# Kernel tuning notes

Measured on AMD Instinct MI355X. Metric: run time of the kernel, lower is better.

The kernel has to match this reference:

```python
import jax, jax.numpy as jnp
import numpy as np

EMB = 128
HID = 256
VOCAB = 32000
B, LS, LT = 16, 256, 128


def _lstm(x_seq, h0, c0, Wk, Wr, b):
    """Keras-style LSTM (gate order i,f,g,o). x_seq: [B,T,D] -> ([B,T,H], h, c)."""
    xz = jnp.einsum('btd,dg->btg', x_seq, Wk) + b  # precompute input projection

    def step(carry, zt):
        h, c = carry
        z = zt + h @ Wr  # [B,4H]
        i, f, g, o = jnp.split(z, 4, axis=-1)
        c = jax.nn.sigmoid(f) * c + jax.nn.sigmoid(i) * jnp.tanh(g)
        h = jax.nn.sigmoid(o) * jnp.tanh(c)
        return (h, c), h

    (h, c), hs = jax.lax.scan(step, (h0, c0), xz.transpose(1, 0, 2))
    return hs.transpose(1, 0, 2), h, c


def setup_inputs() -> dict:
    key = jax.random.key(0)
    ks = jax.random.split(key, 12)
    sd_e = 1.0 / np.sqrt(EMB)
    sd_h = 1.0 / np.sqrt(HID)
    return {
        'x': jax.random.randint(ks[0], (B, LS), 0, VOCAB, dtype=jnp.int32),
        'y': jax.random.randint(ks[1], (B, LT), 0, VOCAB, dtype=jnp.int32),
        'enc_emb': jax.random.normal(ks[2], (VOCAB, EMB), jnp.float32) * 0.05,
        'enc_Wk': jax.random.normal(ks[3], (EMB, 4 * HID), jnp.float32) * sd_e,
        'enc_Wr': jax.random.normal(ks[4], (HID, 4 * HID), jnp.float32) * sd_h,
        'enc_b': jnp.zeros((4 * HID,), jnp.float32),
        'dec_emb': jax.random.normal(ks[5], (VOCAB, EMB), jnp.float32) * 0.05,
        'dec_Wk': jax.random.normal(ks[6], (EMB, 4 * HID), jnp.float32) * sd_e,
        'dec_Wr': jax.random.normal(ks[7], (HID, 4 * HID), jnp.float32) * sd_h,
        'dec_b': jnp.zeros((4 * HID,), jnp.float32),
        'Wout': jax.random.normal(ks[8], (2 * HID, VOCAB), jnp.float32) * (1.0 / np.sqrt(2 * HID)),
        'bout': jnp.zeros((VOCAB,), jnp.float32),
    }


def reference(x, y, enc_emb, enc_Wk, enc_Wr, enc_b, dec_emb, dec_Wk, dec_Wr, dec_b, Wout, bout):
    # ---- Encoder ----
    xe = enc_emb[x]  # [B,LS,EMB]
    z0 = jnp.zeros((x.shape[0], HID), jnp.float32)
    H, h, c = _lstm(xe, z0, z0, enc_Wk, enc_Wr, enc_b)  # H: [B,LS,HID]
    # ---- Decoder (teacher forcing) ----
    ye = dec_emb[y]  # [B,LT,EMB]
    S, hT, cT = _lstm(ye, h, c, dec_Wk, dec_Wr, dec_b)  # [B,LT,HID]
    S_ = jnp.concatenate([h[:, None, :], S[:, :-1, :]], axis=1)  # shifted states
    # Keras Attention (dot, no scale): A = softmax(S_ H^T) H
    scores = jnp.einsum('btd,bsd->bts', S_, H)  # [B,LT,LS]
    A = jnp.einsum('bts,bsd->btd', jax.nn.softmax(scores, axis=-1), H)
    feat = jnp.concatenate([S, A], axis=-1)  # [B,LT,2*HID]
    probs = jax.nn.softmax(feat @ Wout + bout, axis=-1)  # [B,LT,VOCAB]
    return probs
```

## Files before the change

### kernel.cpp

```cpp
#include <hip/hip_runtime.h>
#include <hip/hip_bf16.h>
#include <math.h>

#define BB    16
#define LS    256
#define LT    128
#define EMB   128
#define HID   256
#define G4    1024
#define VOCAB 32000

#define NSL   8
#define XROWS 112

typedef __attribute__((ext_vector_type(8))) short bf16x8;
typedef __attribute__((ext_vector_type(4))) float f32x4;
typedef __attribute__((ext_vector_type(4))) int   i32x4;
typedef unsigned short ushort_t;
typedef unsigned int uint_t;

__device__ inline float sigf(float x)      { return 1.0f / (1.0f + __expf(-x)); }
__device__ inline float tanhfast(float x)  { return 1.0f - 2.0f / (1.0f + __expf(2.0f * x)); }
__device__ inline ushort_t bf16_rne(float f) {
  __hip_bfloat16 h = __float2bfloat16(f);
  return *(ushort_t*)&h;
}

__global__ __launch_bounds__(256) void embed_proj_kernel(
    const int* __restrict__ x, const int* __restrict__ y,
    const float* __restrict__ eemb, const float* __restrict__ eWk,
    const float* __restrict__ eb,
    const float* __restrict__ demb, const float* __restrict__ dWk,
    const float* __restrict__ db,
    float* __restrict__ xze, float* __restrict__ xzd)
{
  const bool enc = blockIdx.x < 128;
  const int* idx = enc ? x : y;
  const float* emb = enc ? eemb : demb;
  const float* Wk  = enc ? eWk  : dWk;
  const float* bias= enc ? eb   : db;
  float* xz        = enc ? xze  : xzd;
  const int row0 = (enc ? blockIdx.x : blockIdx.x - 128) * 32;

  __shared__ float e[32][EMB];
  const int tid = threadIdx.x;

  for (int i = tid; i < 32 * EMB; i += 256) {
    int r = i >> 7, k = i & 127;
    int token = idx[row0 + r];
    e[r][k] = emb[(size_t)token * EMB + k];
  }
  __syncthreads();

  float acc[4][32];
#pragma unroll
  for (int q = 0; q < 4; ++q)
#pragma unroll
    for (int r = 0; r < 32; ++r) acc[q][r] = 0.0f;

  for (int k = 0; k < EMB; ++k) {
    float w0 = Wk[(size_t)k * G4 + 0 * 256 + tid];
    float w1 = Wk[(size_t)k * G4 + 1 * 256 + tid];
    float w2 = Wk[(size_t)k * G4 + 2 * 256 + tid];
    float w3 = Wk[(size_t)k * G4 + 3 * 256 + tid];
#pragma unroll
    for (int r = 0; r < 32; ++r) {
      float ev = e[r][k];
      acc[0][r] = fmaf(ev, w0, acc[0][r]);
      acc[1][r] = fmaf(ev, w1, acc[1][r]);
      acc[2][r] = fmaf(ev, w2, acc[2][r]);
      acc[3][r] = fmaf(ev, w3, acc[3][r]);
    }
  }
#pragma unroll
  for (int q = 0; q < 4; ++q) {
    float bb = bias[q * 256 + tid];
#pragma unroll
    for (int r = 0; r < 32; ++r)
      xz[(size_t)(row0 + r) * G4 + q * 256 + tid] = acc[q][r] + bb;
  }
}

__global__ __launch_bounds__(512, 1) void lstm_kernel(
    const float* __restrict__ xz,
    const float* __restrict__ Wr,
    const float* __restrict__ h0,
    int h0_stride,
    const float* __restrict__ cinit,
    float* __restrict__ Hout,
    float* __restrict__ c_fin,
    i32x4* __restrict__ nmb,
    i32x4* __restrict__ fmb,
    int kid,
    int T)
{
  const int b    = blockIdx.x & (BB - 1);
  const int s    = blockIdx.x >> 4;
  const int tid  = threadIdx.x;
  const int lane = tid & 63;
  const int quarter = tid >> 7;
  const int col  = tid & 127;
  const int gate = col >> 5, u = col & 31;

  __shared__ float part[2][4][128];
  __shared__ float xbuf[XROWS][128];

  float w_r[64];
  {
    const float* wp = Wr + (size_t)(quarter * 64) * G4 + gate * 256 + s * 32 + u;
#pragma unroll
    for (int j = 0; j < 64; ++j) w_r[j] = wp[(size_t)j * G4];
  }

  const int i0 = quarter * 64 + lane;
  float hv = 0.0f;
  if (h0) hv = h0[(size_t)b * h0_stride + i0];

  float cs0 = 0.0f, cs1 = 0.0f;
  if (tid < 16 && cinit) {
    cs0 = cinit[b * HID + s * 32 + 2 * tid];
    cs1 = cinit[b * HID + s * 32 + 2 * tid + 1];
  }

  const int c0i = i0 >> 1;
  const int sel = i0 & 1;

  int tp = XROWS;
  for (int t = 0; t < T; ++t, ++tp) {
    if (tp >= XROWS) {
      __syncthreads();
      tp = 0;
      for (int tt = quarter; tt < XROWS; tt += 4) {
        int ts = t + tt;
        if (ts < T)
          xbuf[tt][col] = xz[((size_t)b * T + ts) * G4 + gate * 256 + s * 32 + u];
      }
    }

    float a0 = 0.0f, a1 = 0.0f, a2 = 0.0f, a3 = 0.0f;
#pragma unroll
    for (int j = 0; j < 64; j += 4) {
      a0 = fmaf(__int_as_float(__builtin_amdgcn_readlane(__float_as_int(hv), j + 0)), w_r[j + 0], a0);
      a1 = fmaf(__int_as_float(__builtin_amdgcn_readlane(__float_as_int(hv), j + 1)), w_r[j + 1], a1);
      a2 = fmaf(__int_as_float(__builtin_amdgcn_readlane(__float_as_int(hv), j + 2)), w_r[j + 2], a2);
      a3 = fmaf(__int_as_float(__builtin_amdgcn_readlane(__float_as_int(hv), j + 3)), w_r[j + 3], a3);
    }
    part[t & 1][quarter][col] = (a0 + a1) + (a2 + a3);
    __syncthreads();

    const int stamp = (t + 1) | (kid << 20);
    const size_t slot = (size_t)(b * 2 + (t & 1)) * 128;

    if (tid < 16) {
      const int ua = 2 * tid, ub = ua + 1;
      const float (*pp)[128] = part[t & 1];
      float p0a = pp[0][ua] + pp[1][ua] + pp[2][ua] + pp[3][ua];
      float p0b = pp[0][ub] + pp[1][ub] + pp[2][ub] + pp[3][ub];
      float p1a = pp[0][32 + ua] + pp[1][32 + ua] + pp[2][32 + ua] + pp[3][32 + ua];
      float p1b = pp[0][32 + ub] + pp[1][32 + ub] + pp[2][32 + ub] + pp[3][32 + ub];
      float p2a = pp[0][64 + ua] + pp[1][64 + ua] + pp[2][64 + ua] + pp[3][64 + ua];
      float p2b = pp[0][64 + ub] + pp[1][64 + ub] + pp[2][64 + ub] + pp[3][64 + ub];
      float p3a = pp[0][96 + ua] + pp[1][96 + ua] + pp[2][96 + ua] + pp[3][96 + ua];
      float p3b = pp[0][96 + ub] + pp[1][96 + ub] + pp[2][96 + ub] + pp[3][96 + ub];
      float2 xg0 = *(const float2*)&xbuf[tp][ua];
      float2 xg1 = *(const float2*)&xbuf[tp][32 + ua];
      float2 xg2 = *(const float2*)&xbuf[tp][64 + ua];
      float2 xg3 = *(const float2*)&xbuf[tp][96 + ua];

      float zi0 = p0a + xg0.x, zi1 = p0b + xg0.y;
      float zf0 = p1a + xg1.x, zf1 = p1b + xg1.y;
      float zg0 = p2a + xg2.x, zg1 = p2b + xg2.y;
      float zo0 = p3a + xg3.x, zo1 = p3b + xg3.y;

      cs0 = fmaf(sigf(zf0), cs0, sigf(zi0) * tanhfast(zg0));
      cs1 = fmaf(sigf(zf1), cs1, sigf(zi1) * tanhfast(zg1));
      float ha = sigf(zo0) * tanhfast(cs0);
      float hb = sigf(zo1) * tanhfast(cs1);

      *(float2*)&Hout[((size_t)b * T + t) * HID + s * 32 + ua] = make_float2(ha, hb);

      i32x4 ch;
      ch.x = __float_as_int(ha);
      ch.y = __float_as_int(hb);
      ch.z = ch.x ^ ch.y ^ stamp;
      ch.w = 0;
      const i32x4* nd = nmb + slot + s * 16 + tid;
      const i32x4* fd = fmb + slot + s * 16 + tid;
      asm volatile("global_store_dwordx4 %0, %1, off sc0"
                   :: "v"(nd), "v"(ch) : "memory");
      asm volatile("global_store_dwordx4 %0, %1, off sc0 sc1"
                   :: "v"(fd), "v"(ch) : "memory");
    }

    if (t + 1 < T) {
      const i32x4* np = nmb + slot + c0i;
      const i32x4* fp = fmb + slot + c0i;
      i32x4 v;
      for (;;) {
        asm volatile("global_load_dwordx4 %0, %1, off sc0\n\t"
                     "s_waitcnt vmcnt(0)"
                     : "=&v"(v) : "v"(np) : "memory");
        if (v.z == (v.x ^ v.y ^ stamp)) break;
        asm volatile("global_load_dwordx4 %0, %1, off sc0 sc1\n\t"
                     "s_waitcnt vmcnt(0)"
                     : "=&v"(v) : "v"(fp) : "memory");
        if (v.z == (v.x ^ v.y ^ stamp)) break;
      }
      hv = __int_as_float(sel ? v.y : v.x);
    }
  }
  if (c_fin && tid < 16)
    *(float2*)&c_fin[b * HID + s * 32 + 2 * tid] = make_float2(cs0, cs1);
}

__global__ __launch_bounds__(256) void mid_kernel(
    const float* __restrict__ W, ushort_t* __restrict__ WT,
    const float* __restrict__ Henc, const float* __restrict__ S,
    __hip_bfloat16* __restrict__ featB)
{
  const int tid = threadIdx.x;

  if (blockIdx.x < 4000) {
    __shared__ float tile[64][65];
    const int nt = blockIdx.x % 500;
    const int kt = blockIdx.x / 500;
    const int n0 = nt * 64, k0 = kt * 64;
    const int r = tid >> 6, c = tid & 63;

#pragma unroll
    for (int q = 0; q < 16; ++q) {
      int kk = q * 4 + r;
      tile[kk][c] = W[(size_t)(k0 + kk) * VOCAB + n0 + c];
    }
    __syncthreads();

    const int nl = tid >> 2;
    const int seg = (tid & 3) * 16;
    uint_t o[8];
#pragma unroll
    for (int j = 0; j < 8; ++j) {
      uint_t lo = bf16_rne(tile[seg + 2 * j][nl]);
      uint_t hi = bf16_rne(tile[seg + 2 * j + 1][nl]);
      o[j] = lo | (hi << 16);
    }
    ushort_t* dst = WT + (size_t)(n0 + nl) * 512 + k0 + seg;
    ((uint4*)dst)[0] = make_uint4(o[0], o[1], o[2], o[3]);
    ((uint4*)dst)[1] = make_uint4(o[4], o[5], o[6], o[7]);
  } else {
    __shared__ float srow[HID];
    __shared__ float p[LS];
    __shared__ float sm[LS];

    const int m = blockIdx.x - 4000;
    const int b = m >> 7, t = m & (LT - 1);

    const float* s_ = (t == 0) ? (Henc + ((size_t)b * LS + (LS - 1)) * HID)
                               : (S + (size_t)(m - 1) * HID);
    srow[tid] = s_[tid];
    __syncthreads();

    const float4* h4 = (const float4*)(Henc + ((size_t)b * LS + tid) * HID);
    const float4* s4 = (const float4*)srow;
    float sc = 0.0f;
#pragma unroll 8
    for (int k = 0; k < HID / 4; ++k) {
      float4 a = h4[k], q = s4[k];
      sc += a.x * q.x + a.y * q.y + a.z * q.z + a.w * q.w;
    }
    sm[tid] = sc;
    __syncthreads();
    for (int st = 128; st > 0; st >>= 1) {
      if (tid < st) sm[tid] = fmaxf(sm[tid], sm[tid + st]);
      __syncthreads();
    }
    float mx = sm[0];
    __syncthreads();
    float e = __expf(sc - mx);
    p[tid] = e;
    sm[tid] = e;
    __syncthreads();
    for (int st = 128; st > 0; st >>= 1) {
      if (tid < st) sm[tid] += sm[tid + st];
      __syncthreads();
    }
    float inv = 1.0f / sm[0];

    float a_d = 0.0f;
#pragma unroll 4
    for (int s2 = 0; s2 < LS; ++s2)
      a_d = fmaf(p[s2], Henc[((size_t)b * LS + s2) * HID + tid], a_d);
    a_d *= inv;

    featB[(size_t)m * (2 * HID) + tid]       = __float2bfloat16(S[(size_t)m * HID + tid]);
    featB[(size_t)m * (2 * HID) + HID + tid] = __float2bfloat16(a_d);
  }
}

__device__ inline void gemm_tile(
    const ushort_t* __restrict__ A, const ushort_t* __restrict__ BT,
    f32x4 (&acc)[8][4], int m0, int n0, int r, int kg)
{
#pragma unroll
  for (int i = 0; i < 8; ++i)
#pragma unroll
    for (int j = 0; j < 4; ++j) acc[i][j] = (f32x4){0.f, 0.f, 0.f, 0.f};

  for (int ks = 0; ks < 16; ++ks) {
    const int kb = ks * 32 + kg * 8;
    bf16x8 a[8], bb[4];
#pragma unroll
    for (int i = 0; i < 8; ++i)
      a[i] = *(const bf16x8*)(A + (size_t)(m0 + i * 16 + r) * 512 + kb);
#pragma unroll
    for (int j = 0; j < 4; ++j)
      bb[j] = *(const bf16x8*)(BT + (size_t)(n0 + j * 16 + r) * 512 + kb);
#pragma unroll
    for (int i = 0; i < 8; ++i)
#pragma unroll
      for (int j = 0; j < 4; ++j)
        acc[i][j] = __builtin_amdgcn_mfma_f32_16x16x32_bf16(a[i], bb[j], acc[i][j], 0, 0, 0);
  }
}

__global__ __launch_bounds__(256) void proj_exp_kernel(
    const ushort_t* __restrict__ A, const ushort_t* __restrict__ BT,
    const float* __restrict__ bout, float* __restrict__ rowsum,
    float* __restrict__ out)
{
  const int k2 = (blockIdx.x & 7) * 250 + (blockIdx.x >> 3);
  const int nt = k2 >> 3;
  const int mt = k2 & 7;
  const int wave = threadIdx.x >> 6, lane = threadIdx.x & 63;
  const int wm = wave >> 1, wn = wave & 1;
  const int r = lane & 15, kg = lane >> 4;
  const int m0 = mt * 256 + wm * 128;
  const int n0 = nt * 128 + wn * 64;

  f32x4 acc[8][4];
  gemm_tile(A, BT, acc, m0, n0, r, kg);

  float bv[4];
#pragma unroll
  for (int j = 0; j < 4; ++j) bv[j] = bout[n0 + j * 16 + r];

#pragma unroll
  for (int i = 0; i < 8; ++i)
#pragma unroll
    for (int q = 0; q < 4; ++q) {
      const int row = m0 + i * 16 + kg * 4 + q;
      float v = 0.0f;
#pragma unroll
      for (int j = 0; j < 4; ++j) {
        float e = __expf(acc[i][j][q] + bv[j]);
        out[(size_t)row * VOCAB + n0 + j * 16 + r] = e;
        v += e;
      }
#pragma unroll
      for (int msk = 1; msk < 16; msk <<= 1) v += __shfl_xor(v, msk, 64);
      if (r == 0) atomicAdd(&rowsum[row], v);
    }
}

__global__ __launch_bounds__(256) void scale_kernel(
    float* __restrict__ out, const float* __restrict__ rowsum)
{
  const int row = blockIdx.x >> 2;
  const int seg = blockIdx.x & 3;
  const float s = 1.0f / rowsum[row];
  float4* o4 = (float4*)(out + (size_t)row * VOCAB) + seg * 2000;
  for (int i = threadIdx.x; i < 2000; i += 256) {
    float4 v = o4[i];
    v.x *= s; v.y *= s; v.z *= s; v.w *= s;
    o4[i] = v;
  }
}

extern "C" void kernel_launch(void* const* d_in, const int* in_sizes, int n_in,
                              void* d_out, int out_size, void* d_ws, size_t ws_size,
                              hipStream_t stream) {
  (void)in_sizes; (void)n_in; (void)out_size; (void)ws_size;

  const int*   x       = (const int*)d_in[0];
  const int*   y       = (const int*)d_in[1];
  const float* enc_emb = (const float*)d_in[2];
  const float* enc_Wk  = (const float*)d_in[3];
  const float* enc_Wr  = (const float*)d_in[4];
  const float* enc_b   = (const float*)d_in[5];
  const float* dec_emb = (const float*)d_in[6];
  const float* dec_Wk  = (const float*)d_in[7];
  const float* dec_Wr  = (const float*)d_in[8];
  const float* dec_b   = (const float*)d_in[9];
  const float* Wout    = (const float*)d_in[10];
  const float* bout    = (const float*)d_in[11];
  float* out = (float*)d_out;
  char*  ws  = (char*)d_ws;

  size_t off = 0;
  float* xz_enc = (float*)(ws + off); off += (size_t)BB * LS * G4 * 4;
  float* xz_dec = (float*)(ws + off); off += (size_t)BB * LT * G4 * 4;
  float* Henc   = (float*)(ws + off); off += (size_t)BB * LS * HID * 4;
  float* S      = (float*)(ws + off); off += (size_t)BB * LT * HID * 4;
  __hip_bfloat16* featB = (__hip_bfloat16*)(ws + off);
  off += (size_t)BB * LT * 2 * HID * 2;
  ushort_t* WoutT = (ushort_t*)(ws + off); off += (size_t)VOCAB * 512 * 2;
  float* c_fin  = (float*)(ws + off); off += (size_t)BB * HID * 4;
  size_t zero_base = off;
  float* rowsum = (float*)(ws + off); off += (size_t)BB * LT * 4;
  i32x4* nmb    = (i32x4*)(ws + off); off += (size_t)BB * 2 * 128 * 16;
  i32x4* fmb    = (i32x4*)(ws + off); off += (size_t)BB * 2 * 128 * 16;
  size_t zero_len = off - zero_base;

  hipMemsetAsync(ws + zero_base, 0, zero_len, stream);

  embed_proj_kernel<<<192, 256, 0, stream>>>(
      x, y, enc_emb, enc_Wk, enc_b, dec_emb, dec_Wk, dec_b, xz_enc, xz_dec);

  lstm_kernel<<<NSL * BB, 512, 0, stream>>>(
      xz_enc, enc_Wr, nullptr, 0, nullptr, Henc, c_fin, nmb, fmb, 0, LS);

  lstm_kernel<<<NSL * BB, 512, 0, stream>>>(
      xz_dec, dec_Wr, Henc + (size_t)(LS - 1) * HID, LS * HID, c_fin,
      S, nullptr, nmb, fmb, 1, LT);

  mid_kernel<<<4000 + BB * LT, 256, 0, stream>>>(
      Wout, WoutT, Henc, S, (__hip_bfloat16*)featB);

  proj_exp_kernel<<<8 * 250, 256, 0, stream>>>(
      (const ushort_t*)featB, WoutT, bout, rowsum, out);
  scale_kernel<<<4 * BB * LT, 256, 0, stream>>>(out, rowsum);
}
```

Measured before the change: 1.283 ms.

## Stage projection GEMM tiles in swizzled LDS and simplify LSTM mailbox sync

The vocab projection GEMM now uses 128x128 block tiles and double-buffers A and B in LDS with an XOR swizzle, instead of having each wave stream operands directly from global memory. This raises operand reuse across the four waves and doubles the grid. Separately, the LSTM inter-block exchange drops the non-coherent mailbox store and poll, keeps only the system-coherent one, and adds a block barrier after the store. The barrier and the loss of the faster mailbox may add latency on the serial recurrent path.

```diff
diff --git a/kernel.cpp b/kernel.cpp
--- a/kernel.cpp
+++ b/kernel.cpp
@@ -89,7 +89,6 @@
     const float* __restrict__ cinit,
     float* __restrict__ Hout,
     float* __restrict__ c_fin,
-    i32x4* __restrict__ nmb,
     i32x4* __restrict__ fmb,
     int kid,
     int T)
@@ -184,23 +183,16 @@
       ch.y = __float_as_int(hb);
       ch.z = ch.x ^ ch.y ^ stamp;
       ch.w = 0;
-      const i32x4* nd = nmb + slot + s * 16 + tid;
       const i32x4* fd = fmb + slot + s * 16 + tid;
-      asm volatile("global_store_dwordx4 %0, %1, off sc0"
-                   :: "v"(nd), "v"(ch) : "memory");
       asm volatile("global_store_dwordx4 %0, %1, off sc0 sc1"
                    :: "v"(fd), "v"(ch) : "memory");
     }
+    __syncthreads();
 
     if (t + 1 < T) {
-      const i32x4* np = nmb + slot + c0i;
       const i32x4* fp = fmb + slot + c0i;
       i32x4 v;
       for (;;) {
-        asm volatile("global_load_dwordx4 %0, %1, off sc0\n\t"
-                     "s_waitcnt vmcnt(0)"
-                     : "=&v"(v) : "v"(np) : "memory");
-        if (v.z == (v.x ^ v.y ^ stamp)) break;
         asm volatile("global_load_dwordx4 %0, %1, off sc0 sc1\n\t"
                      "s_waitcnt vmcnt(0)"
                      : "=&v"(v) : "v"(fp) : "memory");
@@ -296,63 +288,90 @@
   }
 }
 
-__device__ inline void gemm_tile(
-    const ushort_t* __restrict__ A, const ushort_t* __restrict__ BT,
-    f32x4 (&acc)[8][4], int m0, int n0, int r, int kg)
-{
-#pragma unroll
-  for (int i = 0; i < 8; ++i)
-#pragma unroll
-    for (int j = 0; j < 4; ++j) acc[i][j] = (f32x4){0.f, 0.f, 0.f, 0.f};
-
-  for (int ks = 0; ks < 16; ++ks) {
-    const int kb = ks * 32 + kg * 8;
-    bf16x8 a[8], bb[4];
-#pragma unroll
-    for (int i = 0; i < 8; ++i)
-      a[i] = *(const bf16x8*)(A + (size_t)(m0 + i * 16 + r) * 512 + kb);
-#pragma unroll
-    for (int j = 0; j < 4; ++j)
-      bb[j] = *(const bf16x8*)(BT + (size_t)(n0 + j * 16 + r) * 512 + kb);
-#pragma unroll
-    for (int i = 0; i < 8; ++i)
-#pragma unroll
-      for (int j = 0; j < 4; ++j)
-        acc[i][j] = __builtin_amdgcn_mfma_f32_16x16x32_bf16(a[i], bb[j], acc[i][j], 0, 0, 0);
-  }
-}
-
 __global__ __launch_bounds__(256) void proj_exp_kernel(
     const ushort_t* __restrict__ A, const ushort_t* __restrict__ BT,
     const float* __restrict__ bout, float* __restrict__ rowsum,
     float* __restrict__ out)
 {
-  const int k2 = (blockIdx.x & 7) * 250 + (blockIdx.x >> 3);
-  const int nt = k2 >> 3;
-  const int mt = k2 & 7;
-  const int wave = threadIdx.x >> 6, lane = threadIdx.x & 63;
+  __shared__ ushort_t Ab[2][128 * 64];
+  __shared__ ushort_t Bb[2][128 * 64];
+
+  const int bid = blockIdx.x;
+  const int k2 = (bid & 7) * 500 + (bid >> 3);
+  const int mt = k2 & 15, nt = k2 >> 4;
+  const int m0 = mt * 128, n0 = nt * 128;
+  const int tid = threadIdx.x;
+  const int wave = tid >> 6, lane = tid & 63;
   const int wm = wave >> 1, wn = wave & 1;
   const int r = lane & 15, kg = lane >> 4;
-  const int m0 = mt * 256 + wm * 128;
-  const int n0 = nt * 128 + wn * 64;
-
-  f32x4 acc[8][4];
-  gemm_tile(A, BT, acc, m0, n0, r, kg);
+
+  const ushort_t* Ag = A + (size_t)m0 * 512;
+  const ushort_t* Bg = BT + (size_t)n0 * 512;
+
+  f32x4 acc[4][4];
+#pragma unroll
+  for (int i = 0; i < 4; ++i)
+#pragma unroll
+    for (int j = 0; j < 4; ++j) acc[i][j] = (f32x4){0.f, 0.f, 0.f, 0.f};
+
+#define STAGE(kc, buf)                                                       \
+  {                                                                          \
+    _Pragma("unroll")                                                        \
+    for (int q = 0; q < 4; ++q) {                                            \
+      int L = q * 256 + tid;                                                 \
+      int row_ = L >> 3, seg_ = L & 7;                                       \
+      int so_ = row_ * 64 + ((seg_ ^ (row_ & 7)) << 3);                      \
+      uint4 va_ = *(const uint4*)(Ag + (size_t)row_ * 512 + (kc) * 64 + seg_ * 8); \
+      uint4 vb_ = *(const uint4*)(Bg + (size_t)row_ * 512 + (kc) * 64 + seg_ * 8); \
+      *(uint4*)&Ab[buf][so_] = va_;                                          \
+      *(uint4*)&Bb[buf][so_] = vb_;                                          \
+    }                                                                        \
+  }
+
+  STAGE(0, 0);
+  __syncthreads();
+
+  for (int kc = 0; kc < 8; ++kc) {
+    const int cur = kc & 1;
+    if (kc < 7) STAGE(kc + 1, cur ^ 1);
+#pragma unroll
+    for (int ks = 0; ks < 2; ++ks) {
+      bf16x8 a[4], b[4];
+      const int seg = ks * 4 + kg;
+#pragma unroll
+      for (int i = 0; i < 4; ++i) {
+        int row = wm * 64 + i * 16 + r;
+        a[i] = *(const bf16x8*)&Ab[cur][row * 64 + ((seg ^ (row & 7)) << 3)];
+      }
+#pragma unroll
+      for (int j = 0; j < 4; ++j) {
+        int row = wn * 64 + j * 16 + r;
+        b[j] = *(const bf16x8*)&Bb[cur][row * 64 + ((seg ^ (row & 7)) << 3)];
+      }
+#pragma unroll
+      for (int i = 0; i < 4; ++i)
+#pragma unroll
+        for (int j = 0; j < 4; ++j)
+          acc[i][j] = __builtin_amdgcn_mfma_f32_16x16x32_bf16(a[i], b[j], acc[i][j], 0, 0, 0);
+    }
+    __syncthreads();
+  }
+#undef STAGE
 
   float bv[4];
 #pragma unroll
-  for (int j = 0; j < 4; ++j) bv[j] = bout[n0 + j * 16 + r];
-
-#pragma unroll
-  for (int i = 0; i < 8; ++i)
+  for (int j = 0; j < 4; ++j) bv[j] = bout[n0 + wn * 64 + j * 16 + r];
+
+#pragma unroll
+  for (int i = 0; i < 4; ++i)
 #pragma unroll
     for (int q = 0; q < 4; ++q) {
-      const int row = m0 + i * 16 + kg * 4 + q;
+      const int row = m0 + wm * 64 + i * 16 + kg * 4 + q;
       float v = 0.0f;
 #pragma unroll
       for (int j = 0; j < 4; ++j) {
         float e = __expf(acc[i][j][q] + bv[j]);
-        out[(size_t)row * VOCAB + n0 + j * 16 + r] = e;
+        out[(size_t)row * VOCAB + n0 + wn * 64 + j * 16 + r] = e;
         v += e;
       }
 #pragma unroll
@@ -406,7 +425,6 @@
   float* c_fin  = (float*)(ws + off); off += (size_t)BB * HID * 4;
   size_t zero_base = off;
   float* rowsum = (float*)(ws + off); off += (size_t)BB * LT * 4;
-  i32x4* nmb    = (i32x4*)(ws + off); off += (size_t)BB * 2 * 128 * 16;
   i32x4* fmb    = (i32x4*)(ws + off); off += (size_t)BB * 2 * 128 * 16;
   size_t zero_len = off - zero_base;
 
@@ -416,16 +434,16 @@
       x, y, enc_emb, enc_Wk, enc_b, dec_emb, dec_Wk, dec_b, xz_enc, xz_dec);
 
   lstm_kernel<<<NSL * BB, 512, 0, stream>>>(
-      xz_enc, enc_Wr, nullptr, 0, nullptr, Henc, c_fin, nmb, fmb, 0, LS);
+      xz_enc, enc_Wr, nullptr, 0, nullptr, Henc, c_fin, fmb, 0, LS);
 
   lstm_kernel<<<NSL * BB, 512, 0, stream>>>(
       xz_dec, dec_Wr, Henc + (size_t)(LS - 1) * HID, LS * HID, c_fin,
-      S, nullptr, nmb, fmb, 1, LT);
+      S, nullptr, fmb, 1, LT);
 
   mid_kernel<<<4000 + BB * LT, 256, 0, stream>>>(
       Wout, WoutT, Henc, S, (__hip_bfloat16*)featB);
 
-  proj_exp_kernel<<<8 * 250, 256, 0, stream>>>(
+  proj_exp_kernel<<<16 * 250, 256, 0, stream>>>(
       (const ushort_t*)featB, WoutT, bout, rowsum, out);
   scale_kernel<<<4 * BB * LT, 256, 0, stream>>>(out, rowsum);
 }
```

Measured after the change: 1.099 ms. 14.4% less time.
